# Optimization experiments

Hardware: AMD Instinct MI355X
Metric: run time of the kernel (lower is better)

The kernel has to match this reference:

```python
import jax, jax.numpy as jnp
import numpy as np
from jax import lax

B, LEN_SEQ, D_MODEL, N_HEAD, FACTOR, D_FF = 16, 512, 512, 8, 5, 2048
EPS = 1e-5


def layer_norm(x):
    mu = x.mean(-1, keepdims=True)
    var = ((x - mu) ** 2).mean(-1, keepdims=True)
    return (x - mu) * lax.rsqrt(var + EPS)


def pos_encode(x):
    pos = jnp.arange(LEN_SEQ, dtype=jnp.float32)[:, None]
    div = jnp.exp(jnp.arange(0, D_MODEL, 2, dtype=jnp.float32) * (-np.log(10000.0) / D_MODEL))
    pe = jnp.zeros((LEN_SEQ, D_MODEL))
    pe = pe.at[:, 0::2].set(jnp.sin(pos * div)).at[:, 1::2].set(jnp.cos(pos * div))
    return x + pe[None]


def prob_attention(Q, K, V, rkey):
    # Q,K,V: [B,H,L,D]; Informer ProbSparse attention, mask_flag=False
    Bq, H, L_Q, D = Q.shape
    L_K = K.shape[2]
    U_part = min(FACTOR * int(np.ceil(np.log(L_K))), L_K)   # sampled keys per query
    u = min(FACTOR * int(np.ceil(np.log(L_Q))), L_Q)        # top queries kept
    idx = jax.random.randint(rkey, (L_Q, U_part), 0, L_K)
    K_samp = K[:, :, idx, :]                                # [B,H,L_Q,U_part,D]
    QK_samp = jnp.einsum('bhld,bhlsd->bhls', Q, K_samp)
    M = QK_samp.max(-1) - QK_samp.sum(-1) / L_K             # sparsity measure
    _, top = lax.top_k(M, u)                                # [B,H,u]
    Q_red = jnp.take_along_axis(Q, top[..., None], axis=2)  # [B,H,u,D]
    scores = jnp.einsum('bhud,bhkd->bhuk', Q_red, K) * (1.0 / np.sqrt(D))
    upd = jnp.einsum('bhuk,bhkd->bhud', jax.nn.softmax(scores, -1), V)
    ctx = jnp.broadcast_to(V.mean(2, keepdims=True), (Bq, H, L_Q, D))
    bi = jnp.arange(Bq)[:, None, None]
    hi = jnp.arange(H)[None, :, None]
    return ctx.at[bi, hi, top].set(upd)


def setup_inputs():
    key = jax.random.key(0)
    ks = jax.random.split(key, 12)
    s = 0.02
    d, f = D_MODEL, D_FF
    n = jax.random.normal
    return {
        'input_data': n(ks[0], (B, LEN_SEQ, d), jnp.float32),
        'Wq': n(ks[1], (d, d)) * s, 'bq': jnp.zeros((d,)),
        'Wk': n(ks[2], (d, d)) * s, 'bk': jnp.zeros((d,)),
        'Wv': n(ks[3], (d, d)) * s, 'bv': jnp.zeros((d,)),
        'Wo': n(ks[4], (d, d)) * s, 'bo': jnp.zeros((d,)),
        'enc_w1': n(ks[5], (d, f)) * s, 'enc_b1': jnp.zeros((f,)),
        'enc_w2': n(ks[6], (f, d)) * s, 'enc_b2': jnp.zeros((d,)),
        'dec_w1': n(ks[7], (d, f)) * s, 'dec_b1': jnp.zeros((f,)),
        'dec_w2': n(ks[8], (f, d)) * s, 'dec_b2': jnp.zeros((d,)),
        'dist_w': n(ks[9], (d, d, 3)) * s, 'dist_b': jnp.zeros((d,)),
        'out_w': n(ks[10], (d, 1)) * s, 'out_b': jnp.zeros((1,)),
    }


def reference(input_data, Wq, bq, Wk, bk, Wv, bv, Wo, bo,
              enc_w1, enc_b1, enc_w2, enc_b2,
              dec_w1, dec_b1, dec_w2, dec_b2,
              dist_w, dist_b, out_w, out_b):
    base = jax.random.key(42)

    def attn(q_in, k_in, v_in, i):
        Bq, L, _ = q_in.shape
        S = k_in.shape[1]
        Q = (q_in @ Wq + bq).reshape(Bq, L, N_HEAD, -1).transpose(0, 2, 1, 3)
        K = (k_in @ Wk + bk).reshape(Bq, S, N_HEAD, -1).transpose(0, 2, 1, 3)
        V = (v_in @ Wv + bv).reshape(Bq, S, N_HEAD, -1).transpose(0, 2, 1, 3)
        ctx = prob_attention(Q, K, V, jax.random.fold_in(base, i))
        return ctx.transpose(0, 2, 1, 3).reshape(Bq, L, -1) @ Wo + bo

    def encoder(x, i):
        x = layer_norm(x + attn(x, x, x, i))
        y = jax.nn.relu(x @ enc_w1 + enc_b1) @ enc_w2 + enc_b2
        return layer_norm(x + y)

    def distill(x):  # conv1d(circular) + batchnorm + ELU + maxpool(3,2,1)
        xc = x.transpose(0, 2, 1)                                   # [B,d,L]
        xp = jnp.concatenate([xc[..., -1:], xc, xc[..., :1]], -1)   # circular pad
        y = lax.conv_general_dilated(xp, dist_w, (1,), 'VALID',
                                     dimension_numbers=('NCH', 'OIH', 'NCH'))
        y = y + dist_b[None, :, None]
        mu = y.mean((0, 2), keepdims=True)
        var = ((y - mu) ** 2).mean((0, 2), keepdims=True)
        y = jax.nn.elu((y - mu) * lax.rsqrt(var + EPS))
        y = lax.reduce_window(y, -jnp.inf, lax.max, (1, 1, 3), (1, 1, 2),
                              [(0, 0), (0, 0), (1, 1)])
        return y.transpose(0, 2, 1)

    enc_inp = pos_encode(input_data)
    dec_inp = pos_encode(input_data)
    e = distill(encoder(enc_inp, 0))   # 512 -> 256
    e = distill(encoder(e, 1))         # 256 -> 128
    e = distill(encoder(e, 2))         # 128 -> 64
    # decoder (source DecoderLayer never applies its norms; dropout = identity in eval)
    out1 = dec_inp + attn(dec_inp, dec_inp, dec_inp, 3)
    out2 = out1 + attn(out1, e, e, 4)
    y = jax.nn.relu(out2 @ dec_w1 + dec_b1) @ dec_w2 + dec_b2
    out3 = y + out2
    return out3 @ out_w + out_b
```

## Files before the change

### kernel.cpp

```cpp
#include <hip/hip_runtime.h>
#include <cstdint>
#include <cmath>


#define HD __host__ __device__

typedef short short8 __attribute__((ext_vector_type(8)));
typedef float float4v __attribute__((ext_vector_type(4)));

__device__ inline short f2bf(float f) {
    unsigned u = __float_as_uint(f);
    unsigned r = u + 0x7FFFu + ((u >> 16) & 1u);
    return (short)(r >> 16);
}

HD inline unsigned rotl32(unsigned x, int r) { return (x << r) | (x >> (32 - r)); }
HD inline void tfround(unsigned& x0, unsigned& x1, int r) {
    x0 += x1; x1 = rotl32(x1, r); x1 ^= x0;
}
HD inline void threefry2x32(unsigned k0, unsigned k1, unsigned c0, unsigned c1,
                            unsigned& o0, unsigned& o1) {
    unsigned ks2 = k0 ^ k1 ^ 0x1BD11BDAu;
    unsigned x0 = c0 + k0, x1 = c1 + k1;
    tfround(x0, x1, 13); tfround(x0, x1, 15); tfround(x0, x1, 26); tfround(x0, x1, 6);
    x0 += k1; x1 += ks2 + 1u;
    tfround(x0, x1, 17); tfround(x0, x1, 29); tfround(x0, x1, 16); tfround(x0, x1, 24);
    x0 += ks2; x1 += k0 + 2u;
    tfround(x0, x1, 13); tfround(x0, x1, 15); tfround(x0, x1, 26); tfround(x0, x1, 6);
    x0 += k0; x1 += k1 + 3u;
    tfround(x0, x1, 17); tfround(x0, x1, 29); tfround(x0, x1, 16); tfround(x0, x1, 24);
    x0 += k1; x1 += ks2 + 4u;
    tfround(x0, x1, 13); tfround(x0, x1, 15); tfround(x0, x1, 26); tfround(x0, x1, 6);
    x0 += ks2; x1 += k0 + 5u;
    o0 = x0; o1 = x1;
}


__global__ void pe_add_k(const float* __restrict__ in, float* __restrict__ out,
                         short* __restrict__ outb, int total) {
    int t = blockIdx.x * 256 + threadIdx.x;
    if (t >= total) return;
    int d = t % 512;
    int l = (t / 512) % 512;
    float i2 = (float)(d & ~1);
    float div = expf(i2 * (-0.017988946039016f));
    float ang = (float)l * div;
    float v = (d & 1) ? cosf(ang) : sinf(ang);
    float r = in[t] + v;
    out[t] = r;
    outb[t] = f2bf(r);
}

__global__ __launch_bounds__(256) void transpose_bf16_k(const float* __restrict__ in,
                                                        short* __restrict__ out, int K, int N) {
    __shared__ float tile[32][33];
    int k0 = blockIdx.y * 32, n0 = blockIdx.x * 32;
    int c = threadIdx.x & 31, r0 = threadIdx.x >> 5;
    for (int rr = r0; rr < 32; rr += 8)
        tile[rr][c] = in[(size_t)(k0 + rr) * N + n0 + c];
    __syncthreads();
    for (int rr = r0; rr < 32; rr += 8)
        out[(size_t)(n0 + rr) * K + k0 + c] = f2bf(tile[c][rr]);
}

__global__ void w2t_k(const float* __restrict__ dw, short* __restrict__ out, int total) {
    int t = blockIdx.x * 256 + threadIdx.x;
    if (t >= total) return;
    int kk = t % 1536;
    int o = t / 1536;
    int h = kk / 512, i = kk % 512;
    out[t] = f2bf(dw[(size_t)o * 1536 + i * 3 + h]);
}

__global__ void bcat_k(const float* __restrict__ b0, const float* __restrict__ b1,
                       const float* __restrict__ b2, float* __restrict__ out) {
    int t = blockIdx.x * 256 + threadIdx.x;
    if (t >= 1536) return;
    out[t] = (t < 512) ? b0[t] : (t < 1024 ? b1[t - 512] : b2[t - 1024]);
}

__device__ inline void swizzle_bid(int bid, int nbx, int nby, int& bm, int& bn) {
    if ((nby & 7) == 0) {
        int stripe = nby >> 3;
        int x = bid & 7, w = bid >> 3;
        bn = w % nbx;
        bm = x * stripe + w / nbx;
    } else {
        bn = bid % nbx;
        bm = bid / nbx;
    }
}

__global__ __launch_bounds__(256) void gemm128_k(
    const short* __restrict__ A, const short* __restrict__ Bt,
    const float* __restrict__ bias, const float* __restrict__ res,
    float* __restrict__ C32, short* __restrict__ C16,
    int M, int N, int K, int relu, int ldC) {
    __shared__ short As[128 * 40];
    __shared__ short Bs[128 * 40];
    int tid = threadIdx.x;
    int wave = tid >> 6, lane = tid & 63;
    int wy = wave >> 1, wx = wave & 1;
    int rl = lane & 15, quad = lane >> 4;
    int bm, bn;
    swizzle_bid(blockIdx.x, N >> 7, M >> 7, bm, bn);
    bm <<= 7; bn <<= 7;

    float4v acc[4][4];
    #pragma unroll
    for (int i = 0; i < 4; i++)
        #pragma unroll
        for (int j = 0; j < 4; j++) acc[i][j] = (float4v){0.f, 0.f, 0.f, 0.f};

    for (int k0 = 0; k0 < K; k0 += 32) {
        #pragma unroll
        for (int it = 0; it < 2; it++) {
            int c = tid + it * 256;
            int row = c >> 2, seg = c & 3;
            *(float4*)&As[row * 40 + seg * 8] =
                *(const float4*)(A + (size_t)(bm + row) * K + k0 + seg * 8);
        }
        #pragma unroll
        for (int it = 0; it < 2; it++) {
            int c = tid + it * 256;
            int row = c >> 2, seg = c & 3;
            *(float4*)&Bs[row * 40 + seg * 8] =
                *(const float4*)(Bt + (size_t)(bn + row) * K + k0 + seg * 8);
        }
        __syncthreads();
        short8 a[4], b[4];
        #pragma unroll
        for (int i = 0; i < 4; i++)
            a[i] = *(const short8*)&As[(wy * 64 + i * 16 + rl) * 40 + quad * 8];
        #pragma unroll
        for (int j = 0; j < 4; j++)
            b[j] = *(const short8*)&Bs[(wx * 64 + j * 16 + rl) * 40 + quad * 8];
        #pragma unroll
        for (int i = 0; i < 4; i++)
            #pragma unroll
            for (int j = 0; j < 4; j++)
                acc[i][j] = __builtin_amdgcn_mfma_f32_16x16x32_bf16(a[i], b[j], acc[i][j], 0, 0, 0);
        __syncthreads();
    }
    #pragma unroll
    for (int i = 0; i < 4; i++) {
        #pragma unroll
        for (int r = 0; r < 4; r++) {
            int gm = bm + wy * 64 + i * 16 + quad * 4 + r;
            #pragma unroll
            for (int j = 0; j < 4; j++) {
                int gn = bn + wx * 64 + j * 16 + rl;
                float v = acc[i][j][r];
                if (bias) v += bias[gn];
                if (relu) v = fmaxf(v, 0.f);
                if (res) v += res[(size_t)gm * ldC + gn];
                if (C32) C32[(size_t)gm * ldC + gn] = v;
                if (C16) C16[(size_t)gm * ldC + gn] = f2bf(v);
            }
        }
    }
}

__global__ __launch_bounds__(256) void gemm64_k(
    const short* __restrict__ A, const short* __restrict__ Bt,
    const float* __restrict__ bias, const float* __restrict__ res,
    float* __restrict__ C32, short* __restrict__ C16,
    int M, int N, int K, int relu, int ldC) {
    __shared__ short As[64 * 40];
    __shared__ short Bs[64 * 40];
    int tid = threadIdx.x;
    int wave = tid >> 6, lane = tid & 63;
    int rl = lane & 15, quad = lane >> 4;
    int bm, bn;
    swizzle_bid(blockIdx.x, N >> 6, M >> 6, bm, bn);
    bm <<= 6; bn <<= 6;

    float4v acc[4];
    #pragma unroll
    for (int j = 0; j < 4; j++) acc[j] = (float4v){0.f, 0.f, 0.f, 0.f};

    int row = tid >> 2, seg = tid & 3;
    for (int k0 = 0; k0 < K; k0 += 32) {
        *(float4*)&As[row * 40 + seg * 8] =
            *(const float4*)(A + (size_t)(bm + row) * K + k0 + seg * 8);
        *(float4*)&Bs[row * 40 + seg * 8] =
            *(const float4*)(Bt + (size_t)(bn + row) * K + k0 + seg * 8);
        __syncthreads();
        short8 a = *(const short8*)&As[(wave * 16 + rl) * 40 + quad * 8];
        short8 b[4];
        #pragma unroll
        for (int j = 0; j < 4; j++)
            b[j] = *(const short8*)&Bs[(j * 16 + rl) * 40 + quad * 8];
        #pragma unroll
        for (int j = 0; j < 4; j++)
            acc[j] = __builtin_amdgcn_mfma_f32_16x16x32_bf16(a, b[j], acc[j], 0, 0, 0);
        __syncthreads();
    }
    #pragma unroll
    for (int r = 0; r < 4; r++) {
        int gm = bm + wave * 16 + quad * 4 + r;
        #pragma unroll
        for (int j = 0; j < 4; j++) {
            int gn = bn + j * 16 + rl;
            float v = acc[j][r];
            if (bias) v += bias[gn];
            if (relu) v = fmaxf(v, 0.f);
            if (res) v += res[(size_t)gm * ldC + gn];
            if (C32) C32[(size_t)gm * ldC + gn] = v;
            if (C16) C16[(size_t)gm * ldC + gn] = f2bf(v);
        }
    }
}

__global__ void ridx_k(unsigned k0, unsigned k1, int size, unsigned mask, int* __restrict__ idx) {
    int j = blockIdx.x * 256 + threadIdx.x;
    if (j >= size) return;
    unsigned o0, o1;
    threefry2x32(k0, k1, (unsigned)j, (unsigned)(j + size), o0, o1);
    idx[j] = (int)(o1 & mask);
}

extern __shared__ float kslab[];
__global__ __launch_bounds__(256) void msamp_lds_k(
    const float* __restrict__ Qp, const float* __restrict__ Kp,
    const int* __restrict__ idx, float* __restrict__ Mout,
    int LQ, int LK, int U, int ld) {
    int bid = blockIdx.x;
    int half = bid & 1;
    int bh = bid >> 1;
    int h = bh & 7, b = bh >> 3;
    const float* kbase = Kp + (size_t)b * LK * ld + h * 64;
    for (int t = threadIdx.x; t < LK * 16; t += 256) {
        int r = t >> 4, seg = t & 15;
        float4 v = *(const float4*)(kbase + (size_t)r * ld + seg * 4);
        float* dst = &kslab[r * 65 + seg * 4];
        dst[0] = v.x; dst[1] = v.y; dst[2] = v.z; dst[3] = v.w;
    }
    __syncthreads();
    int halfL = LQ >> 1;
    for (int li = threadIdx.x; li < halfL; li += 256) {
        int l = half * halfL + li;
        const float4* q = (const float4*)(Qp + (size_t)(b * LQ + l) * ld + h * 64);
        float qr[64];
        #pragma unroll
        for (int d4 = 0; d4 < 16; d4++) {
            float4 v = q[d4];
            qr[4 * d4] = v.x; qr[4 * d4 + 1] = v.y; qr[4 * d4 + 2] = v.z; qr[4 * d4 + 3] = v.w;
        }
        const int* ip = idx + l * U;
        float mx = -INFINITY, sm = 0.f;
        for (int s = 0; s < U; s++) {
            const float* kr = &kslab[ip[s] * 65];
            float acc = 0.f;
            #pragma unroll
            for (int d = 0; d < 64; d++) acc += qr[d] * kr[d];
            mx = fmaxf(mx, acc);
            sm += acc;
        }
        Mout[(size_t)bh * LQ + l] = mx - sm / (float)LK;
    }
}

__global__ void msamp_k(const float* __restrict__ Qp, const float* __restrict__ Kp,
                        const int* __restrict__ idx, float* __restrict__ Mout,
                        int LQ, int LK, int U, int ld) {
    int t = blockIdx.x * 256 + threadIdx.x;
    int total = 16 * 8 * LQ * 4;
    if (t >= total) return;
    int p = t & 3;
    int rest = t >> 2;
    int l = rest % LQ;
    int h = (rest / LQ) & 7;
    int b = rest / (LQ * 8);
    const float4* q = (const float4*)(Qp + ((size_t)(b * LQ + l) * ld + h * 64));
    const float* kb = Kp + ((size_t)b * LK * ld + h * 64);
    float4 qr[16];
    #pragma unroll
    for (int d = 0; d < 16; d++) qr[d] = q[d];
    float mx = -INFINITY, sm = 0.f;
    for (int s = p; s < U; s += 4) {
        const float4* kr = (const float4*)(kb + (size_t)idx[l * U + s] * ld);
        float acc = 0.f;
        #pragma unroll
        for (int d = 0; d < 16; d++) {
            float4 kv = kr[d];
            acc += qr[d].x * kv.x + qr[d].y * kv.y + qr[d].z * kv.z + qr[d].w * kv.w;
        }
        mx = fmaxf(mx, acc);
        sm += acc;
    }
    mx = fmaxf(mx, __shfl_xor(mx, 1));
    mx = fmaxf(mx, __shfl_xor(mx, 2));
    sm += __shfl_xor(sm, 1);
    sm += __shfl_xor(sm, 2);
    if (p == 0)
        Mout[(size_t)((b * 8) + h) * LQ + l] = mx - sm / (float)LK;
}

__global__ __launch_bounds__(256) void topk_k(const float* __restrict__ M,
                                              int* __restrict__ top, int LQ, int u) {
    __shared__ float vals[512];
    __shared__ float rv[256];
    __shared__ int ri[256];
    int bh = blockIdx.x;
    int tid = threadIdx.x;
    const float* m = M + (size_t)bh * LQ;
    for (int l = tid; l < LQ; l += 256) vals[l] = m[l];
    __syncthreads();
    for (int j = 0; j < u; j++) {
        float best = -INFINITY;
        int bi = LQ;
        for (int l = tid; l < LQ; l += 256) {
            float v = vals[l];
            if (v > best) { best = v; bi = l; }
        }
        rv[tid] = best; ri[tid] = bi;
        __syncthreads();
        for (int s = 128; s > 0; s >>= 1) {
            if (tid < s) {
                float v2 = rv[tid + s]; int i2 = ri[tid + s];
                if (v2 > rv[tid] || (v2 == rv[tid] && i2 < ri[tid])) { rv[tid] = v2; ri[tid] = i2; }
            }
            __syncthreads();
        }
        int sel = ri[0];
        if (tid == 0) {
            top[bh * u + j] = sel;
            vals[sel] = -INFINITY;
        }
        __syncthreads();
    }
}

__global__ __launch_bounds__(256) void vmean_k(const float* __restrict__ Vp,
                                               float* __restrict__ vm, int LK, int ld) {
    __shared__ float red[8][33];
    int b = blockIdx.y;
    int c0 = blockIdx.x * 32;
    int ci = threadIdx.x & 31, g = threadIdx.x >> 5;
    const float* base = Vp + (size_t)b * LK * ld + c0 + ci;
    float s = 0.f;
    for (int l = g; l < LK; l += 8) s += base[(size_t)l * ld];
    red[g][ci] = s;
    __syncthreads();
    if (threadIdx.x < 32) {
        float t = 0.f;
        #pragma unroll
        for (int g2 = 0; g2 < 8; g2++) t += red[g2][threadIdx.x];
        vm[b * 512 + c0 + threadIdx.x] = t / (float)LK;
    }
}

__global__ void ctx_fill_k(const float* __restrict__ vm, short* __restrict__ ctxb,
                           int LQ, int total) {
    int t = blockIdx.x * 256 + threadIdx.x;
    if (t >= total) return;
    int c = t % 512;
    int b = t / (512 * LQ);
    ctxb[t] = f2bf(vm[b * 512 + c]);
}

__global__ __launch_bounds__(256) void attn_flash_k(
    const float* __restrict__ Qp, const float* __restrict__ Kp, const float* __restrict__ Vp,
    const int* __restrict__ top, short* __restrict__ ctxb, int LQ, int LK, int u, int ld) {
    __shared__ float qs[18][64];
    __shared__ int ls[18];
    __shared__ float kv[64][65];
    __shared__ float sc[18][512];
    int bid = blockIdx.x;
    int chunk = bid & 1;
    int h = (bid >> 1) & 7;
    int b = bid >> 4;
    int CH = (u + 1) >> 1;
    int r0 = chunk * CH;
    int nr = min(CH, u - r0);
    int tid = threadIdx.x;
    int wave = tid >> 6, lane = tid & 63;

    if (tid < nr) ls[tid] = top[((b * 8) + h) * u + r0 + tid];
    __syncthreads();
    for (int t = tid; t < nr * 16; t += 256) {
        int r = t >> 4, seg = t & 15;
        float4 v = *(const float4*)(Qp + ((size_t)(b * LQ + ls[r])) * ld + h * 64 + seg * 4);
        float* dst = &qs[r][seg * 4];
        dst[0] = v.x; dst[1] = v.y; dst[2] = v.z; dst[3] = v.w;
    }

    int ntile = LK >> 6;
    const float* kbase = Kp + ((size_t)b * LK) * ld + h * 64;
    for (int T = 0; T < ntile; T++) {
        __syncthreads();
        #pragma unroll
        for (int it = 0; it < 4; it++) {
            int t = tid + it * 256;
            int kk = t >> 4, seg = t & 15;
            float4 v = *(const float4*)(kbase + (size_t)(T * 64 + kk) * ld + seg * 4);
            float* dst = &kv[kk][seg * 4];
            dst[0] = v.x; dst[1] = v.y; dst[2] = v.z; dst[3] = v.w;
        }
        __syncthreads();
        for (int p = tid; p < nr * 64; p += 256) {
            int r = p >> 6, kk = p & 63;
            float acc = 0.f;
            #pragma unroll
            for (int d = 0; d < 64; d++) acc += qs[r][d] * kv[kk][d];
            sc[r][T * 64 + kk] = acc * 0.125f;
        }
    }
    __syncthreads();
    for (int r = wave; r < nr; r += 4) {
        float mx = -INFINITY;
        for (int k = lane; k < LK; k += 64) mx = fmaxf(mx, sc[r][k]);
        #pragma unroll
        for (int o = 32; o > 0; o >>= 1) mx = fmaxf(mx, __shfl_xor(mx, o));
        float s = 0.f;
        for (int k = lane; k < LK; k += 64) {
            float e = expf(sc[r][k] - mx);
            sc[r][k] = e;
            s += e;
        }
        #pragma unroll
        for (int o = 32; o > 0; o >>= 1) s += __shfl_xor(s, o);
        float inv = 1.0f / s;
        for (int k = lane; k < LK; k += 64) sc[r][k] *= inv;
    }
    float acc[5];
    #pragma unroll
    for (int i = 0; i < 5; i++) acc[i] = 0.f;
    const float* vbase = Vp + ((size_t)b * LK) * ld + h * 64;
    for (int T = 0; T < ntile; T++) {
        __syncthreads();
        #pragma unroll
        for (int it = 0; it < 4; it++) {
            int t = tid + it * 256;
            int kk = t >> 4, seg = t & 15;
            float4 v = *(const float4*)(vbase + (size_t)(T * 64 + kk) * ld + seg * 4);
            float* dst = &kv[kk][seg * 4];
            dst[0] = v.x; dst[1] = v.y; dst[2] = v.z; dst[3] = v.w;
        }
        __syncthreads();
        int ri = 0;
        for (int r = wave; r < nr; r += 4, ri++) {
            float a = 0.f;
            #pragma unroll
            for (int kk = 0; kk < 64; kk++) a += sc[r][T * 64 + kk] * kv[kk][lane];
            acc[ri] += a;
        }
    }
    int ri = 0;
    for (int r = wave; r < nr; r += 4, ri++)
        ctxb[((size_t)(b * LQ + ls[r])) * 512 + h * 64 + lane] = f2bf(acc[ri]);
}

__global__ __launch_bounds__(256) void ln_k(const float* __restrict__ in,
                                            float* __restrict__ out, short* __restrict__ outb) {
    __shared__ float red[256];
    int r = blockIdx.x;
    int tid = threadIdx.x;
    const float* x = in + (size_t)r * 512;
    float a = x[tid], b = x[tid + 256];
    red[tid] = a + b;
    __syncthreads();
    for (int s = 128; s > 0; s >>= 1) {
        if (tid < s) red[tid] += red[tid + s];
        __syncthreads();
    }
    float mu = red[0] / 512.f;
    __syncthreads();
    float d1 = a - mu, d2 = b - mu;
    red[tid] = d1 * d1 + d2 * d2;
    __syncthreads();
    for (int s = 128; s > 0; s >>= 1) {
        if (tid < s) red[tid] += red[tid + s];
        __syncthreads();
    }
    float inv = 1.0f / sqrtf(red[0] / 512.f + 1e-5f);
    float v1 = d1 * inv, v2 = d2 * inv;
    out[(size_t)r * 512 + tid] = v1;
    out[(size_t)r * 512 + tid + 256] = v2;
    if (outb) {
        outb[(size_t)r * 512 + tid] = f2bf(v1);
        outb[(size_t)r * 512 + tid + 256] = f2bf(v2);
    }
}

__global__ void xcat_k(const float* __restrict__ x, short* __restrict__ xc, int L, int total) {
    int t = blockIdx.x * 256 + threadIdx.x;
    if (t >= total) return;
    int i = t % 512;
    int h = (t / 512) % 3;
    int bt = t / 1536;
    int tt = bt % L;
    int b = bt / L;
    int src = (tt + h - 1 + L) % L;
    xc[t] = f2bf(x[(size_t)(b * L + src) * 512 + i]);
}

__global__ __launch_bounds__(256) void bnpart_k(const float* __restrict__ y,
                                                float* __restrict__ ps, float* __restrict__ pq,
                                                int rows) {
    int chunk = blockIdx.x;
    int rpc = rows >> 7;
    int r0 = chunk * rpc;
    int tid = threadIdx.x;
    float s0 = 0.f, s1 = 0.f, q0 = 0.f, q1 = 0.f;
    for (int r = r0; r < r0 + rpc; r++) {
        float a = y[(size_t)r * 512 + tid];
        float b = y[(size_t)r * 512 + tid + 256];
        s0 += a; q0 += a * a;
        s1 += b; q1 += b * b;
    }
    ps[chunk * 512 + tid] = s0;
    ps[chunk * 512 + tid + 256] = s1;
    pq[chunk * 512 + tid] = q0;
    pq[chunk * 512 + tid + 256] = q1;
}

__global__ void bnfin_k(const float* __restrict__ ps, const float* __restrict__ pq,
                        float* __restrict__ mu, float* __restrict__ var, int rows) {
    int o = blockIdx.x * 256 + threadIdx.x;
    if (o >= 512) return;
    float s = 0.f, q = 0.f;
    for (int c = 0; c < 128; c++) {
        s += ps[c * 512 + o];
        q += pq[c * 512 + o];
    }
    float m = s / (float)rows;
    mu[o] = m;
    var[o] = q / (float)rows - m * m;
}

__global__ void elu_pool_k(const float* __restrict__ y, const float* __restrict__ mu,
                           const float* __restrict__ var, float* __restrict__ out,
                           short* __restrict__ outb, int L, int total) {
    int t = blockIdx.x * 256 + threadIdx.x;
    if (t >= total) return;
    int o = t % 512;
    int tp = (t / 512) % (L / 2);
    int b = t / (512 * (L / 2));
    float mm = mu[o];
    float inv = 1.0f / sqrtf(var[o] + 1e-5f);
    float m = -INFINITY;
    #pragma unroll
    for (int dt = 0; dt < 3; dt++) {
        int tt = 2 * tp - 1 + dt;
        if (tt < 0 || tt >= L) continue;
        float v = (y[(size_t)(b * L + tt) * 512 + o] - mm) * inv;
        m = fmaxf(m, v);
    }
    float r = m > 0.f ? m : expm1f(m);
    out[t] = r;
    outb[t] = f2bf(r);
}

__global__ void final_k(const float* __restrict__ x, const float* __restrict__ w,
                        const float* __restrict__ bb, float* __restrict__ out, int rows) {
    int gid = blockIdx.x * 256 + threadIdx.x;
    int wid = gid >> 6;
    int lane = gid & 63;
    if (wid >= rows) return;
    const float* xr = x + (size_t)wid * 512;
    float acc = 0.f;
    for (int k = lane; k < 512; k += 64) acc += xr[k] * w[k];
    for (int off = 32; off > 0; off >>= 1) acc += __shfl_down(acc, off);
    if (lane == 0) out[wid] = acc + bb[0];
}


static inline int iceil_log(int L) { return (int)ceil(log((double)L)); }
static inline int imin(int a, int b) { return a < b ? a : b; }

extern "C" void kernel_launch(void* const* d_in, const int* in_sizes, int n_in,
                              void* d_out, int out_size, void* d_ws, size_t ws_size,
                              hipStream_t stream) {
    const float* IN  = (const float*)d_in[0];
    const float* Wq  = (const float*)d_in[1];
    const float* bq  = (const float*)d_in[2];
    const float* Wk  = (const float*)d_in[3];
    const float* bk  = (const float*)d_in[4];
    const float* Wv  = (const float*)d_in[5];
    const float* bv  = (const float*)d_in[6];
    const float* Wo  = (const float*)d_in[7];
    const float* bo  = (const float*)d_in[8];
    const float* ew1 = (const float*)d_in[9];
    const float* eb1 = (const float*)d_in[10];
    const float* ew2 = (const float*)d_in[11];
    const float* eb2 = (const float*)d_in[12];
    const float* dw1 = (const float*)d_in[13];
    const float* db1 = (const float*)d_in[14];
    const float* dw2 = (const float*)d_in[15];
    const float* db2 = (const float*)d_in[16];
    const float* DW  = (const float*)d_in[17];
    const float* db  = (const float*)d_in[18];
    const float* ow  = (const float*)d_in[19];
    const float* ob  = (const float*)d_in[20];
    float* OUT = (float*)d_out;

    float* ws = (float*)d_ws;
    size_t off = 0;
    auto alloc = [&](size_t n) { float* p = ws + off; off += n; return p; };
    float* PE   = alloc(4194304);
    short* PEb  = (short*)alloc(2097152);
    float* QKV  = alloc(12582912);
    float* CTX  = alloc(4194304);
    short* CTXb = (short*)alloc(2097152);
    float* T1   = alloc(4194304);
    short* T1b  = (short*)alloc(2097152);
    float* XLN  = alloc(4194304);
    short* XLNb = (short*)alloc(2097152);
    float* T2   = alloc(4194304);
    short* T2b  = (short*)alloc(2097152);
    float* T3   = alloc(4194304);
    short* HIDb = (short*)alloc(8388608);
    float* D1   = alloc(2097152);
    short* D1b  = (short*)alloc(1048576);
    float* D2   = alloc(1048576);
    short* D2b  = (short*)alloc(524288);
    short* Ebb  = (short*)alloc(262144);
    float* Ebf  = alloc(524288);
    float* MB   = alloc(65536);
    float* VM   = alloc(8192);
    float* MU   = alloc(512);
    float* VARb = alloc(512);
    float* BQKV = alloc(1536);
    float* PS   = alloc(65536);
    float* PQ   = alloc(65536);
    int* IDX  = (int*)alloc(17920);
    int* TOPB = (int*)alloc(4480);
    short* WqkvT = (short*)alloc(393216);
    short* WoT   = (short*)alloc(131072);
    short* ew1T  = (short*)alloc(524288);
    short* ew2T  = (short*)alloc(524288);
    short* dw1T  = (short*)alloc(524288);
    short* dw2T  = (short*)alloc(524288);
    short* W2T   = (short*)alloc(393216);
    (void)ws_size; (void)n_in; (void)in_sizes; (void)out_size;

    static_assert(512 * 65 * 4 == 133120, "");
    hipError_t attr_ok = hipFuncSetAttribute(
        (const void*)msamp_lds_k, hipFuncAttributeMaxDynamicSharedMemorySize, 133120);

    auto gemm128 = [&](const short* A, const short* Bt, const float* bias, const float* res,
                       float* C32, short* C16, int M, int N, int K, int relu, int ldC) {
        gemm128_k<<<(N / 128) * (M / 128), 256, 0, stream>>>(A, Bt, bias, res, C32, C16,
                                                             M, N, K, relu, ldC);
    };
    auto gemm64 = [&](const short* A, const short* Bt, const float* bias, const float* res,
                      float* C32, short* C16, int M, int N, int K, int relu, int ldC) {
        gemm64_k<<<(N / 64) * (M / 64), 256, 0, stream>>>(A, Bt, bias, res, C32, C16,
                                                          M, N, K, relu, ldC);
    };
    auto tr = [&](const float* W, short* Wt, int K, int N) {
        dim3 g(N / 32, K / 32);
        transpose_bf16_k<<<g, 256, 0, stream>>>(W, Wt, K, N);
    };

    auto attn = [&](const short* qinb, const short* kvinb, const float* resp,
                    float* out32, short* out16, int LQ, int LK, int ikey) {
        int Mq = 16 * LQ, Mk = 16 * LK;
        const int ld = 1536;
        float* Qp = QKV;
        float* Kp = QKV + 512;
        float* Vp = QKV + 1024;
        if (qinb == kvinb) {
            gemm128(qinb, WqkvT, BQKV, nullptr, QKV, nullptr, Mq, 1536, 512, 0, ld);
        } else {
            gemm64(qinb, WqkvT, BQKV, nullptr, QKV, nullptr, Mq, 512, 512, 0, ld);
            gemm64(kvinb, WqkvT + 512 * 512, BQKV + 512, nullptr, QKV + 512, nullptr,
                   Mk, 1024, 512, 0, ld);
        }
        int U = imin(5 * iceil_log(LK), LK);
        int u = imin(5 * iceil_log(LQ), LQ);
        unsigned rk0, rk1;
        threefry2x32(0u, 42u, 0u, (unsigned)ikey, rk0, rk1);
        int size = LQ * U;
        ridx_k<<<(size + 255) / 256, 256, 0, stream>>>(rk0, rk1, size, (unsigned)(LK - 1), IDX);
        size_t shbytes = (size_t)LK * 65 * 4;
        if (attr_ok == hipSuccess || shbytes <= 65536) {
            msamp_lds_k<<<16 * 8 * 2, 256, shbytes, stream>>>(Qp, Kp, IDX, MB, LQ, LK, U, ld);
        } else {
            int totM = 16 * 8 * LQ * 4;
            msamp_k<<<(totM + 255) / 256, 256, 0, stream>>>(Qp, Kp, IDX, MB, LQ, LK, U, ld);
        }
        topk_k<<<128, 256, 0, stream>>>(MB, TOPB, LQ, u);
        vmean_k<<<dim3(16, 16), 256, 0, stream>>>(Vp, VM, LK, ld);
        int totC = 16 * LQ * 512;
        ctx_fill_k<<<(totC + 255) / 256, 256, 0, stream>>>(VM, CTXb, LQ, totC);
        attn_flash_k<<<16 * 8 * 2, 256, 0, stream>>>(Qp, Kp, Vp, TOPB, CTXb, LQ, LK, u, ld);
        gemm64(CTXb, WoT, bo, resp, out32, out16, Mq, 512, 512, 0, 512);
    };

    auto encoder = [&](const short* Xb, const float* X, int L, int ikey, float* OUTenc) {
        int M = 16 * L;
        attn(Xb, Xb, X, T1, nullptr, L, L, ikey);
        ln_k<<<M, 256, 0, stream>>>(T1, XLN, XLNb);
        gemm128(XLNb, ew1T, eb1, nullptr, nullptr, HIDb, M, 2048, 512, 1, 2048);
        gemm64(HIDb, ew2T, eb2, XLN, T2, nullptr, M, 512, 2048, 0, 512);
        ln_k<<<M, 256, 0, stream>>>(T2, OUTenc, nullptr);
    };

    auto distill = [&](const float* X, int L, float* OUTd, short* OUTdb) {
        int M = 16 * L;
        int tot = M * 1536;
        xcat_k<<<(tot + 255) / 256, 256, 0, stream>>>(X, HIDb, L, tot);
        gemm64(HIDb, W2T, db, nullptr, CTX, nullptr, M, 512, 1536, 0, 512);
        bnpart_k<<<128, 256, 0, stream>>>(CTX, PS, PQ, M);
        bnfin_k<<<2, 256, 0, stream>>>(PS, PQ, MU, VARb, M);
        int toto = 16 * (L / 2) * 512;
        elu_pool_k<<<(toto + 255) / 256, 256, 0, stream>>>(CTX, MU, VARb, OUTd, OUTdb, L, toto);
    };

    tr(Wq, WqkvT, 512, 512);
    tr(Wk, WqkvT + 512 * 512, 512, 512);
    tr(Wv, WqkvT + 1024 * 512, 512, 512);
    tr(Wo, WoT, 512, 512);
    tr(ew1, ew1T, 512, 2048);
    tr(ew2, ew2T, 2048, 512);
    tr(dw1, dw1T, 512, 2048);
    tr(dw2, dw2T, 2048, 512);
    w2t_k<<<(786432 + 255) / 256, 256, 0, stream>>>(DW, W2T, 786432);
    bcat_k<<<6, 256, 0, stream>>>(bq, bk, bv, BQKV);

    int totPE = 16 * 512 * 512;
    pe_add_k<<<(totPE + 255) / 256, 256, 0, stream>>>(IN, PE, PEb, totPE);

    encoder(PEb, PE, 512, 0, T3); distill(T3, 512, D1, D1b);
    encoder(D1b, D1, 256, 1, T3); distill(T3, 256, D2, D2b);
    encoder(D2b, D2, 128, 2, T3); distill(T3, 128, Ebf, Ebb);

    attn(PEb, PEb, PE, T1, T1b, 512, 512, 3);
    attn(T1b, Ebb, T1, T2, T2b, 512, 64, 4);
    gemm128(T2b, dw1T, db1, nullptr, nullptr, HIDb, 8192, 2048, 512, 1, 2048);
    gemm64(HIDb, dw2T, db2, T2, T3, nullptr, 8192, 512, 2048, 0, 512);
    final_k<<<(8192 * 64) / 256, 256, 0, stream>>>(T3, ow, ob, OUT, 8192);
}
```

Before: 1.611 ms.

## Use direct global-to-LDS loads in GEMM and add 128x64 tile kernel

```diff
diff --git a/kernel.cpp b/kernel.cpp
--- a/kernel.cpp
+++ b/kernel.cpp
@@ -7,6 +7,13 @@
 
 typedef short short8 __attribute__((ext_vector_type(8)));
 typedef float float4v __attribute__((ext_vector_type(4)));
+
+typedef __attribute__((address_space(1))) const void gvoid;
+typedef __attribute__((address_space(3))) void lvoid;
+
+__device__ __forceinline__ void gl_lds16(const void* g, void* l) {
+    __builtin_amdgcn_global_load_lds((gvoid*)g, (lvoid*)l, 16, 0, 0);
+}
 
 __device__ inline short f2bf(float f) {
     unsigned u = __float_as_uint(f);
@@ -96,8 +103,8 @@
     const float* __restrict__ bias, const float* __restrict__ res,
     float* __restrict__ C32, short* __restrict__ C16,
     int M, int N, int K, int relu, int ldC) {
-    __shared__ short As[128 * 40];
-    __shared__ short Bs[128 * 40];
+    __shared__ short As[128 * 32];
+    __shared__ short Bs[128 * 32];
     int tid = threadIdx.x;
     int wave = tid >> 6, lane = tid & 63;
     int wy = wave >> 1, wx = wave & 1;
@@ -106,6 +113,17 @@
     swizzle_bid(blockIdx.x, N >> 7, M >> 7, bm, bn);
     bm <<= 7; bn <<= 7;
 
+    int srow = (wave << 5) + (lane >> 2);
+    int skol = (lane & 3) << 3;
+    const short* ga0 = A + (size_t)(bm + srow) * K + skol;
+    const short* ga1 = ga0 + (size_t)16 * K;
+    const short* gb0 = Bt + (size_t)(bn + srow) * K + skol;
+    const short* gb1 = gb0 + (size_t)16 * K;
+    short* la0 = &As[wave << 10];
+    short* la1 = la0 + 512;
+    short* lb0 = &Bs[wave << 10];
+    short* lb1 = lb0 + 512;
+
     float4v acc[4][4];
     #pragma unroll
     for (int i = 0; i < 4; i++)
@@ -113,28 +131,18 @@
         for (int j = 0; j < 4; j++) acc[i][j] = (float4v){0.f, 0.f, 0.f, 0.f};
 
     for (int k0 = 0; k0 < K; k0 += 32) {
-        #pragma unroll
-        for (int it = 0; it < 2; it++) {
-            int c = tid + it * 256;
-            int row = c >> 2, seg = c & 3;
-            *(float4*)&As[row * 40 + seg * 8] =
-                *(const float4*)(A + (size_t)(bm + row) * K + k0 + seg * 8);
-        }
-        #pragma unroll
-        for (int it = 0; it < 2; it++) {
-            int c = tid + it * 256;
-            int row = c >> 2, seg = c & 3;
-            *(float4*)&Bs[row * 40 + seg * 8] =
-                *(const float4*)(Bt + (size_t)(bn + row) * K + k0 + seg * 8);
-        }
+        gl_lds16(ga0 + k0, la0);
+        gl_lds16(ga1 + k0, la1);
+        gl_lds16(gb0 + k0, lb0);
+        gl_lds16(gb1 + k0, lb1);
         __syncthreads();
         short8 a[4], b[4];
         #pragma unroll
         for (int i = 0; i < 4; i++)
-            a[i] = *(const short8*)&As[(wy * 64 + i * 16 + rl) * 40 + quad * 8];
+            a[i] = *(const short8*)&As[(wy * 64 + i * 16 + rl) * 32 + quad * 8];
         #pragma unroll
         for (int j = 0; j < 4; j++)
-            b[j] = *(const short8*)&Bs[(wx * 64 + j * 16 + rl) * 40 + quad * 8];
+            b[j] = *(const short8*)&Bs[(wx * 64 + j * 16 + rl) * 32 + quad * 8];
         #pragma unroll
         for (int i = 0; i < 4; i++)
             #pragma unroll
@@ -150,6 +158,75 @@
             #pragma unroll
             for (int j = 0; j < 4; j++) {
                 int gn = bn + wx * 64 + j * 16 + rl;
+                float v = acc[i][j][r];
+                if (bias) v += bias[gn];
+                if (relu) v = fmaxf(v, 0.f);
+                if (res) v += res[(size_t)gm * ldC + gn];
+                if (C32) C32[(size_t)gm * ldC + gn] = v;
+                if (C16) C16[(size_t)gm * ldC + gn] = f2bf(v);
+            }
+        }
+    }
+}
+
+__global__ __launch_bounds__(256) void gemm12864_k(
+    const short* __restrict__ A, const short* __restrict__ Bt,
+    const float* __restrict__ bias, const float* __restrict__ res,
+    float* __restrict__ C32, short* __restrict__ C16,
+    int M, int N, int K, int relu, int ldC) {
+    __shared__ short As[128 * 32];
+    __shared__ short Bs[64 * 32];
+    int tid = threadIdx.x;
+    int wave = tid >> 6, lane = tid & 63;
+    int wy = wave >> 1, wx = wave & 1;
+    int rl = lane & 15, quad = lane >> 4;
+    int bm, bn;
+    swizzle_bid(blockIdx.x, N >> 6, M >> 7, bm, bn);
+    bm <<= 7; bn <<= 6;
+
+    int arow = (wave << 5) + (lane >> 2);
+    int brow = (wave << 4) + (lane >> 2);
+    int skol = (lane & 3) << 3;
+    const short* ga0 = A + (size_t)(bm + arow) * K + skol;
+    const short* ga1 = ga0 + (size_t)16 * K;
+    const short* gb0 = Bt + (size_t)(bn + brow) * K + skol;
+    short* la0 = &As[wave << 10];
+    short* la1 = la0 + 512;
+    short* lb0 = &Bs[wave << 9];
+
+    float4v acc[4][2];
+    #pragma unroll
+    for (int i = 0; i < 4; i++)
+        #pragma unroll
+        for (int j = 0; j < 2; j++) acc[i][j] = (float4v){0.f, 0.f, 0.f, 0.f};
+
+    for (int k0 = 0; k0 < K; k0 += 32) {
+        gl_lds16(ga0 + k0, la0);
+        gl_lds16(ga1 + k0, la1);
+        gl_lds16(gb0 + k0, lb0);
+        __syncthreads();
+        short8 a[4], b[2];
+        #pragma unroll
+        for (int i = 0; i < 4; i++)
+            a[i] = *(const short8*)&As[(wy * 64 + i * 16 + rl) * 32 + quad * 8];
+        #pragma unroll
+        for (int j = 0; j < 2; j++)
+            b[j] = *(const short8*)&Bs[(wx * 32 + j * 16 + rl) * 32 + quad * 8];
+        #pragma unroll
+        for (int i = 0; i < 4; i++)
+            #pragma unroll
+            for (int j = 0; j < 2; j++)
+                acc[i][j] = __builtin_amdgcn_mfma_f32_16x16x32_bf16(a[i], b[j], acc[i][j], 0, 0, 0);
+        __syncthreads();
+    }
+    #pragma unroll
+    for (int i = 0; i < 4; i++) {
+        #pragma unroll
+        for (int r = 0; r < 4; r++) {
+            int gm = bm + wy * 64 + i * 16 + quad * 4 + r;
+            #pragma unroll
+            for (int j = 0; j < 2; j++) {
+                int gn = bn + wx * 32 + j * 16 + rl;
                 float v = acc[i][j][r];
                 if (bias) v += bias[gn];
                 if (relu) v = fmaxf(v, 0.f);
@@ -647,8 +724,13 @@
     };
     auto gemm64 = [&](const short* A, const short* Bt, const float* bias, const float* res,
                       float* C32, short* C16, int M, int N, int K, int relu, int ldC) {
-        gemm64_k<<<(N / 64) * (M / 64), 256, 0, stream>>>(A, Bt, bias, res, C32, C16,
-                                                          M, N, K, relu, ldC);
+        if (M >= 8192 && (M & 127) == 0 && (N & 63) == 0) {
+            gemm12864_k<<<(N / 64) * (M / 128), 256, 0, stream>>>(A, Bt, bias, res, C32, C16,
+                                                                  M, N, K, relu, ldC);
+        } else {
+            gemm64_k<<<(N / 64) * (M / 64), 256, 0, stream>>>(A, Bt, bias, res, C32, C16,
+                                                              M, N, K, relu, ldC);
+        }
     };
     auto tr = [&](const float* W, short* Wt, int K, int N) {
         dim3 g(N / 32, K / 32);
```

Result: no change. 1.624 ms (+0.8%).
